# Kernel tuning notes

Measured on AMD Instinct MI355X. Metric: run time of the kernel, lower is better.

The kernel has to match this reference:

```python
import jax, jax.numpy as jnp
import numpy as np

N = 50000
E = 1600000
H, C = 4, 32
NEG_SLOPE = 0.2
EPS = 1e-16


def _l2norm_row(a):
    # F.normalize(a, p=2, dim=1) for a of shape [1, F]
    return a / jnp.maximum(jnp.linalg.norm(a, axis=1, keepdims=True), 1e-12)


def setup_inputs() -> dict:
    key = jax.random.key(0)
    ks = jax.random.split(key, 7)
    x = jax.random.normal(ks[0], (N, 256), dtype=jnp.float32)
    edge_index = jax.random.randint(ks[1], (2, E), 0, N, dtype=jnp.int32)
    v_mapping = jax.random.normal(ks[2], (64, 256), dtype=jnp.float32) * 0.1
    W_src = jax.random.normal(ks[3], (256, H * C), dtype=jnp.float32) * 0.06
    att_src = jax.random.normal(ks[4], (1, 64), dtype=jnp.float32)
    att_dst = jax.random.normal(ks[5], (1, 64), dtype=jnp.float32)
    bias = jnp.zeros((H * C,), dtype=jnp.float32)
    return {"x": x, "edge_index": edge_index, "v_mapping": v_mapping,
            "W_src": W_src, "att_src": att_src, "att_dst": att_dst, "bias": bias}


def reference(x, edge_index, v_mapping, W_src, att_src, att_dst, bias):
    # node projection: [N, H, C]
    x_proj = (x @ W_src).reshape(-1, H, C)
    # attention-locator scores: scalar per node
    score = x @ v_mapping.T                      # [N, F]
    a_src = (score * _l2norm_row(att_src)).sum(-1)  # [N]
    a_dst = (score * _l2norm_row(att_dst)).sum(-1)  # [N]

    src, dst = edge_index[0], edge_index[1]
    alpha = a_src[src] + a_dst[dst]              # [E]
    alpha = jax.nn.leaky_relu(alpha, NEG_SLOPE)
    # segment softmax over destination nodes
    m = jax.ops.segment_max(alpha, dst, num_segments=N)
    alpha = jnp.exp(alpha - jax.lax.stop_gradient(m)[dst])
    denom = jax.ops.segment_sum(alpha, dst, num_segments=N)
    alpha = alpha / (denom[dst] + EPS)           # [E]

    msg = x_proj[src] * alpha[:, None, None]     # [E, H, C]
    agg = jax.ops.segment_sum(msg, dst, num_segments=N)  # [N, H, C]

    out = x_proj + agg                           # residual as in forward
    out = out.reshape(-1, H * C) + bias          # concat heads + bias
    return out
```

## Files before the change

kernel.cpp:

```cpp
#include <hip/hip_runtime.h>

#define N_NODES 50000
#define E_EDGES 1600000
#define HC 128
#define NEG_SLOPE 0.2f
#define SM_EPS 1e-16f
#define NBKT 391
#define BKT_STRIDE 4800
#define EPB1 4096
#define NB1 391

typedef __attribute__((ext_vector_type(8))) short short8v;
typedef __attribute__((ext_vector_type(4))) float f32x4;

__device__ inline unsigned bf16pack(float a, float b) {
  unsigned ua = __float_as_uint(a), ub = __float_as_uint(b);
  ua = (ua + 0x7fffu + ((ua >> 16) & 1u)) >> 16;
  ub = (ub + 0x7fffu + ((ub >> 16) & 1u)) >> 16;
  return ua | (ub << 16);
}

__global__ __launch_bounds__(256) void k0_init(
    const float* __restrict__ v_mapping,
    const float* __restrict__ att_src,
    const float* __restrict__ att_dst,
    const float* __restrict__ W,
    unsigned short* __restrict__ wT,
    int* __restrict__ gcursor) {
  const int tid = threadIdx.x, bid = blockIdx.x;
  if (bid == 0)
    for (int i = tid; i < NBKT; i += 256) gcursor[i] = i * BKT_STRIDE;

  __shared__ float wv[2][256];
  {
    const int j = tid;
    float ns = 0.f, nd = 0.f;
    for (int f = 0; f < 64; ++f) {
      float a = att_src[f]; ns = fmaf(a, a, ns);
      float b = att_dst[f]; nd = fmaf(b, b, nd);
    }
    ns = fmaxf(sqrtf(ns), 1e-12f);
    nd = fmaxf(sqrtf(nd), 1e-12f);
    float s = 0.f, d = 0.f;
    for (int f = 0; f < 64; ++f) {
      float v = v_mapping[f * 256 + j];
      s = fmaf(v, att_src[f], s);
      d = fmaf(v, att_dst[f], d);
    }
    wv[0][j] = s / ns;
    wv[1][j] = d / nd;
  }
  __syncthreads();

#pragma unroll
  for (int r = 0; r < 8; ++r) {
    const int n = bid * 8 + r;
    const int k = tid;
    float v;
    if (n < 128) v = W[k * 128 + n];
    else if (n == 128) v = wv[0][k];
    else if (n == 129) v = wv[1][k];
    else v = 0.f;
    unsigned u = __float_as_uint(v);
    u = (u + 0x7fffu + ((u >> 16) & 1u)) >> 16;
    wT[n * 256 + k] = (unsigned short)u;
  }
}

__global__ __launch_bounds__(256) void k1_node(
    const float* __restrict__ x,
    const unsigned short* __restrict__ wT,
    unsigned* __restrict__ xpb,
    float* __restrict__ a_src, float* __restrict__ a_dst) {
  __shared__ unsigned short xs[64 * 264];
  const int tid = threadIdx.x;
  const int w = tid >> 6, lane = tid & 63;
  const int rowbase = blockIdx.x * 64;

  const float4* x4 = (const float4*)x;
#pragma unroll
  for (int c = 0; c < 16; ++c) {
    const int idx = c * 256 + tid;
    const int row = idx >> 6, c4 = idx & 63;
    float4 v = make_float4(0.f, 0.f, 0.f, 0.f);
    if (rowbase + row < N_NODES) v = x4[(size_t)(rowbase + row) * 64 + c4];
    uint2 p;
    p.x = bf16pack(v.x, v.y);
    p.y = bf16pack(v.z, v.w);
    *(uint2*)&xs[row * 264 + c4 * 4] = p;
  }
  __syncthreads();

  f32x4 acc[9];
#pragma unroll
  for (int t = 0; t < 9; ++t) acc[t] = (f32x4){0.f, 0.f, 0.f, 0.f};

  const int m = lane & 15, kq = lane >> 4;
  const unsigned short* arow = &xs[(w * 16 + m) * 264 + kq * 8];
#pragma unroll
  for (int ks = 0; ks < 8; ++ks) {
    const short8v af = *(const short8v*)(arow + ks * 32);
#pragma unroll
    for (int ct = 0; ct < 9; ++ct) {
      const short8v bf = *(const short8v*)(wT + (ct * 16 + m) * 256 + ks * 32 + kq * 8);
      acc[ct] = __builtin_amdgcn_mfma_f32_16x16x32_bf16(af, bf, acc[ct], 0, 0, 0);
    }
  }

  if (m < 2) {
    float* ap = m ? a_dst : a_src;
#pragma unroll
    for (int i = 0; i < 4; ++i) {
      const int rg = rowbase + w * 16 + kq * 4 + i;
      if (rg < N_NODES) ap[rg] = acc[8][i];
    }
  }

  float* cs = (float*)&xs[w * 16 * 264];
#pragma unroll
  for (int ct = 0; ct < 8; ++ct)
#pragma unroll
    for (int i = 0; i < 4; ++i)
      cs[(kq * 4 + i) * 132 + ct * 16 + m] = acc[ct][i];
  __syncthreads();

  const int prow = lane & 15, q = lane >> 4;
  const int grow = rowbase + w * 16 + prow;
  unsigned uu[16];
#pragma unroll
  for (int u = 0; u < 16; ++u) {
    const float2 f2 = *(const float2*)&cs[prow * 132 + q * 32 + u * 2];
    uu[u] = bf16pack(f2.x, f2.y);
  }
  if (grow < N_NODES) {
    uint4* d4 = (uint4*)&xpb[(size_t)grow * 64 + q * 16];
    d4[0] = make_uint4(uu[0], uu[1], uu[2], uu[3]);
    d4[1] = make_uint4(uu[4], uu[5], uu[6], uu[7]);
    d4[2] = make_uint4(uu[8], uu[9], uu[10], uu[11]);
    d4[3] = make_uint4(uu[12], uu[13], uu[14], uu[15]);
  }
}

__global__ __launch_bounds__(256) void kc1_coarse(
    const int* __restrict__ ei,
    const float* __restrict__ a_src, const float* __restrict__ a_dst,
    int* __restrict__ gcursor, int2* __restrict__ coarse) {
  __shared__ int chist[NBKT];
  __shared__ int gbase[NBKT];
  __shared__ int ccur[NBKT];
  const int tid = threadIdx.x;
  const int ebase = blockIdx.x * EPB1;
  for (int b = tid; b < NBKT; b += 256) { chist[b] = 0; ccur[b] = 0; }
  __syncthreads();

#pragma unroll
  for (int i = 0; i < 16; ++i) {
    const int e = ebase + i * 256 + tid;
    if (e < E_EDGES) atomicAdd(&chist[ei[E_EDGES + e] >> 7], 1);
  }
  __syncthreads();

  for (int b = tid; b < NBKT; b += 256) {
    const int c = chist[b];
    if (c > 0) gbase[b] = atomicAdd(&gcursor[b], c);
  }
  __syncthreads();

#pragma unroll
  for (int i = 0; i < 16; ++i) {
    const int e = ebase + i * 256 + tid;
    if (e < E_EDGES) {
      const int s = ei[e];
      const int d = ei[E_EDGES + e];
      const int b = d >> 7;
      float a = a_src[s] + a_dst[d];
      a = a > 0.f ? a : NEG_SLOPE * a;
      const float ev = __expf(a);
      const int pos = gbase[b] + atomicAdd(&ccur[b], 1);
      if (pos < (b + 1) * BKT_STRIDE)
        coarse[pos] = make_int2(s | ((d & 127) << 16), __float_as_int(ev));
    }
  }
}

__global__ __launch_bounds__(256) void kc2_reduce(
    const int* __restrict__ gcursor, const int2* __restrict__ coarse,
    const unsigned* __restrict__ xpb,
    const float* __restrict__ bias,
    float* __restrict__ out) {
  __shared__ unsigned sorted[BKT_STRIDE];
  __shared__ int hist[128], cur[128];
  __shared__ int base[129];
  const int b = blockIdx.x;
  const int tid = threadIdx.x;
  const int cstart = b * BKT_STRIDE;
  const int cnt = min(gcursor[b] - cstart, BKT_STRIDE);

  if (tid < 128) { hist[tid] = 0; cur[tid] = 0; }
  __syncthreads();

  for (int j = tid; j < cnt; j += 256)
    atomicAdd(&hist[(coarse[cstart + j].x >> 16) & 127], 1);
  __syncthreads();

  if (tid < 64) {
    const int h0 = hist[2 * tid], h1 = hist[2 * tid + 1];
    const int pair = h0 + h1;
    int inc = pair;
#pragma unroll
    for (int off = 1; off < 64; off <<= 1) {
      int t = __shfl_up(inc, off);
      if (tid >= off) inc += t;
    }
    const int excl = inc - pair;
    base[2 * tid] = excl;
    base[2 * tid + 1] = excl + h0;
    if (tid == 63) base[128] = inc;
  }
  __syncthreads();

  for (int j = tid; j < cnt; j += 256) {
    const int2 e2 = coarse[cstart + j];
    const int dloc = (e2.x >> 16) & 127;
    unsigned uev = (unsigned)e2.y;
    uev = (uev + 0x7fffu + ((uev >> 16) & 1u)) >> 16;
    const int p = base[dloc] + atomicAdd(&cur[dloc], 1);
    sorted[p] = (unsigned)(e2.x & 0xffff) | (uev << 16);
  }
  __syncthreads();

  const int g = tid >> 4, gl = tid & 15;
  const uint4* xp4 = (const uint4*)xpb;
  const float4* br = (const float4*)bias;
  const float4 b0 = br[2 * gl], b1 = br[2 * gl + 1];

  for (int dl = g; dl < 128; dl += 16) {
    const int dst = (b << 7) | dl;
    if (dst >= N_NODES) break;
    const int s0 = base[dl];
    const int cntd = base[dl + 1] - s0;

    float acc[8];
#pragma unroll
    for (int i = 0; i < 8; ++i) acc[i] = 0.f;
    float den = 0.f;

    for (int j = 0; j < cntd; ++j) {
      const unsigned u = sorted[s0 + j];
      const float ev = __uint_as_float(u & 0xffff0000u);
      const uint4 v = xp4[(size_t)(u & 0xffffu) * 16 + gl];
      den += ev;
      acc[0] = fmaf(ev, __uint_as_float(v.x << 16), acc[0]);
      acc[1] = fmaf(ev, __uint_as_float(v.x & 0xffff0000u), acc[1]);
      acc[2] = fmaf(ev, __uint_as_float(v.y << 16), acc[2]);
      acc[3] = fmaf(ev, __uint_as_float(v.y & 0xffff0000u), acc[3]);
      acc[4] = fmaf(ev, __uint_as_float(v.z << 16), acc[4]);
      acc[5] = fmaf(ev, __uint_as_float(v.z & 0xffff0000u), acc[5]);
      acc[6] = fmaf(ev, __uint_as_float(v.w << 16), acc[6]);
      acc[7] = fmaf(ev, __uint_as_float(v.w & 0xffff0000u), acc[7]);
    }

    const float inv = 1.f / (den + SM_EPS);
    const uint4 ur = xp4[(size_t)dst * 16 + gl];
    float4 o0, o1;
    o0.x = __uint_as_float(ur.x << 16)         + b0.x + acc[0] * inv;
    o0.y = __uint_as_float(ur.x & 0xffff0000u) + b0.y + acc[1] * inv;
    o0.z = __uint_as_float(ur.y << 16)         + b0.z + acc[2] * inv;
    o0.w = __uint_as_float(ur.y & 0xffff0000u) + b0.w + acc[3] * inv;
    o1.x = __uint_as_float(ur.z << 16)         + b1.x + acc[4] * inv;
    o1.y = __uint_as_float(ur.z & 0xffff0000u) + b1.y + acc[5] * inv;
    o1.z = __uint_as_float(ur.w << 16)         + b1.z + acc[6] * inv;
    o1.w = __uint_as_float(ur.w & 0xffff0000u) + b1.w + acc[7] * inv;
    float4* orow = (float4*)(out + (size_t)dst * HC);
    orow[2 * gl] = o0;
    orow[2 * gl + 1] = o1;
  }
}

extern "C" void kernel_launch(void* const* d_in, const int* in_sizes, int n_in,
                              void* d_out, int out_size, void* d_ws, size_t ws_size,
                              hipStream_t stream) {
  const float* x         = (const float*)d_in[0];
  const int*   ei        = (const int*)d_in[1];
  const float* v_mapping = (const float*)d_in[2];
  const float* W_src     = (const float*)d_in[3];
  const float* att_src   = (const float*)d_in[4];
  const float* att_dst   = (const float*)d_in[5];
  const float* bias      = (const float*)d_in[6];
  float* out = (float*)d_out;

  char* ws = (char*)d_ws;
  unsigned*       xpb     = (unsigned*)ws;        ws += (size_t)N_NODES * 64 * 4;
  float*          a_src   = (float*)ws;           ws += (size_t)N_NODES * 4;
  float*          a_dst   = (float*)ws;           ws += (size_t)N_NODES * 4;
  unsigned short* wT      = (unsigned short*)ws;  ws += 144 * 256 * 2;
  int*            gcursor = (int*)ws;             ws += ((NBKT + 127) / 128) * 128 * 4;
  int2*           coarse  = (int2*)ws;            ws += (size_t)NBKT * BKT_STRIDE * 8;

  k0_init<<<18, 256, 0, stream>>>(v_mapping, att_src, att_dst, W_src, wT, gcursor);
  k1_node<<<(N_NODES + 63) / 64, 256, 0, stream>>>(x, wT, xpb, a_src, a_dst);
  kc1_coarse<<<NB1, 256, 0, stream>>>(ei, a_src, a_dst, gcursor, coarse);
  kc2_reduce<<<NBKT, 256, 0, stream>>>(gcursor, coarse, xpb, bias, out);
}
```

Measured before the change: 157.8 us.

## Halve destination bucket size to 64 nodes and unroll gather loop by two

Destination buckets shrink from 128 to 64 nodes, doubling the number of reduce blocks (782) so more workgroups run in parallel, with less shared memory each and a simpler single-element scan. The per-destination gather loop is unrolled by two so two independent row loads are in flight at once. This trades more global atomics on bucket cursors and a larger coarse histogram in the scatter kernel for better occupancy and memory-level parallelism. The per-bucket stride of 2600 still has to hold the edge count per bucket, which averages about 2048.

```diff
diff --git a/kernel.cpp b/kernel.cpp
--- a/kernel.cpp
+++ b/kernel.cpp
@@ -5,8 +5,8 @@
 #define HC 128
 #define NEG_SLOPE 0.2f
 #define SM_EPS 1e-16f
-#define NBKT 391
-#define BKT_STRIDE 4800
+#define NBKT 782
+#define BKT_STRIDE 2600
 #define EPB1 4096
 #define NB1 391
 
@@ -156,7 +156,7 @@
 #pragma unroll
   for (int i = 0; i < 16; ++i) {
     const int e = ebase + i * 256 + tid;
-    if (e < E_EDGES) atomicAdd(&chist[ei[E_EDGES + e] >> 7], 1);
+    if (e < E_EDGES) atomicAdd(&chist[ei[E_EDGES + e] >> 6], 1);
   }
   __syncthreads();
 
@@ -172,13 +172,13 @@
     if (e < E_EDGES) {
       const int s = ei[e];
       const int d = ei[E_EDGES + e];
-      const int b = d >> 7;
+      const int b = d >> 6;
       float a = a_src[s] + a_dst[d];
       a = a > 0.f ? a : NEG_SLOPE * a;
       const float ev = __expf(a);
       const int pos = gbase[b] + atomicAdd(&ccur[b], 1);
       if (pos < (b + 1) * BKT_STRIDE)
-        coarse[pos] = make_int2(s | ((d & 127) << 16), __float_as_int(ev));
+        coarse[pos] = make_int2(s | ((d & 63) << 16), __float_as_int(ev));
     }
   }
 }
@@ -189,39 +189,36 @@
     const float* __restrict__ bias,
     float* __restrict__ out) {
   __shared__ unsigned sorted[BKT_STRIDE];
-  __shared__ int hist[128], cur[128];
-  __shared__ int base[129];
+  __shared__ int hist[64], cur[64];
+  __shared__ int base[65];
   const int b = blockIdx.x;
   const int tid = threadIdx.x;
   const int cstart = b * BKT_STRIDE;
   const int cnt = min(gcursor[b] - cstart, BKT_STRIDE);
 
-  if (tid < 128) { hist[tid] = 0; cur[tid] = 0; }
+  if (tid < 64) { hist[tid] = 0; cur[tid] = 0; }
   __syncthreads();
 
   for (int j = tid; j < cnt; j += 256)
-    atomicAdd(&hist[(coarse[cstart + j].x >> 16) & 127], 1);
+    atomicAdd(&hist[(coarse[cstart + j].x >> 16) & 63], 1);
   __syncthreads();
 
   if (tid < 64) {
-    const int h0 = hist[2 * tid], h1 = hist[2 * tid + 1];
-    const int pair = h0 + h1;
-    int inc = pair;
+    const int h = hist[tid];
+    int inc = h;
 #pragma unroll
     for (int off = 1; off < 64; off <<= 1) {
       int t = __shfl_up(inc, off);
       if (tid >= off) inc += t;
     }
-    const int excl = inc - pair;
-    base[2 * tid] = excl;
-    base[2 * tid + 1] = excl + h0;
-    if (tid == 63) base[128] = inc;
+    base[tid] = inc - h;
+    if (tid == 63) base[64] = inc;
   }
   __syncthreads();
 
   for (int j = tid; j < cnt; j += 256) {
     const int2 e2 = coarse[cstart + j];
-    const int dloc = (e2.x >> 16) & 127;
+    const int dloc = (e2.x >> 16) & 63;
     unsigned uev = (unsigned)e2.y;
     uev = (uev + 0x7fffu + ((uev >> 16) & 1u)) >> 16;
     const int p = base[dloc] + atomicAdd(&cur[dloc], 1);
@@ -234,8 +231,8 @@
   const float4* br = (const float4*)bias;
   const float4 b0 = br[2 * gl], b1 = br[2 * gl + 1];
 
-  for (int dl = g; dl < 128; dl += 16) {
-    const int dst = (b << 7) | dl;
+  for (int dl = g; dl < 64; dl += 16) {
+    const int dst = (b << 6) | dl;
     if (dst >= N_NODES) break;
     const int s0 = base[dl];
     const int cntd = base[dl + 1] - s0;
@@ -245,7 +242,33 @@
     for (int i = 0; i < 8; ++i) acc[i] = 0.f;
     float den = 0.f;
 
-    for (int j = 0; j < cntd; ++j) {
+    int j = 0;
+    for (; j + 2 <= cntd; j += 2) {
+      const unsigned uA = sorted[s0 + j];
+      const unsigned uB = sorted[s0 + j + 1];
+      const float evA = __uint_as_float(uA & 0xffff0000u);
+      const float evB = __uint_as_float(uB & 0xffff0000u);
+      const uint4 vA = xp4[(size_t)(uA & 0xffffu) * 16 + gl];
+      const uint4 vB = xp4[(size_t)(uB & 0xffffu) * 16 + gl];
+      den += evA + evB;
+      acc[0] = fmaf(evA, __uint_as_float(vA.x << 16), acc[0]);
+      acc[1] = fmaf(evA, __uint_as_float(vA.x & 0xffff0000u), acc[1]);
+      acc[2] = fmaf(evA, __uint_as_float(vA.y << 16), acc[2]);
+      acc[3] = fmaf(evA, __uint_as_float(vA.y & 0xffff0000u), acc[3]);
+      acc[4] = fmaf(evA, __uint_as_float(vA.z << 16), acc[4]);
+      acc[5] = fmaf(evA, __uint_as_float(vA.z & 0xffff0000u), acc[5]);
+      acc[6] = fmaf(evA, __uint_as_float(vA.w << 16), acc[6]);
+      acc[7] = fmaf(evA, __uint_as_float(vA.w & 0xffff0000u), acc[7]);
+      acc[0] = fmaf(evB, __uint_as_float(vB.x << 16), acc[0]);
+      acc[1] = fmaf(evB, __uint_as_float(vB.x & 0xffff0000u), acc[1]);
+      acc[2] = fmaf(evB, __uint_as_float(vB.y << 16), acc[2]);
+      acc[3] = fmaf(evB, __uint_as_float(vB.y & 0xffff0000u), acc[3]);
+      acc[4] = fmaf(evB, __uint_as_float(vB.z << 16), acc[4]);
+      acc[5] = fmaf(evB, __uint_as_float(vB.z & 0xffff0000u), acc[5]);
+      acc[6] = fmaf(evB, __uint_as_float(vB.w << 16), acc[6]);
+      acc[7] = fmaf(evB, __uint_as_float(vB.w & 0xffff0000u), acc[7]);
+    }
+    if (j < cntd) {
       const unsigned u = sorted[s0 + j];
       const float ev = __uint_as_float(u & 0xffff0000u);
       const uint4 v = xp4[(size_t)(u & 0xffffu) * 16 + gl];
```

Measured after the change: 152.2 us. 1.04x faster.
